# Kernel tuning notes

Hardware: AMD Instinct MI355X
Metric: run time of the kernel (lower is better)

Reference implementation:

```python
import jax, jax.numpy as jnp
import numpy as np

N_NODES = 50000
N_EDGES = 800000
C_IN = 64
C_HID = 64
C_OUT = 64


def _glorot(key, shape):
    lim = (6.0 / (shape[0] + shape[1])) ** 0.5
    return jax.random.uniform(key, shape, jnp.float32, -lim, lim)


def setup_inputs() -> dict:
    key = jax.random.key(0)
    ks = jax.random.split(key, 8)
    x = jax.random.normal(ks[0], (N_NODES, C_IN), jnp.float32)
    edge_index = jax.random.randint(ks[1], (2, N_EDGES), 0, N_NODES, jnp.int64)
    return {
        "x": x,
        "edge_index": edge_index,
        # ChebConv layer 1 (K=2): lins[0], lins[1], bias
        "W1_0": _glorot(ks[2], (C_IN, C_HID)),
        "W1_1": _glorot(ks[3], (C_IN, C_HID)),
        "b1": jnp.zeros((C_HID,), jnp.float32),
        # ChebConv layer 2 (K=2)
        "W2_0": _glorot(ks[4], (C_HID, C_OUT)),
        "W2_1": _glorot(ks[5], (C_HID, C_OUT)),
        "b2": jnp.zeros((C_OUT,), jnp.float32),
    }


def _lhat_matvec(x, src, dst, num_nodes):
    """Apply scaled Laplacian L_hat = -D^{-1/2} A D^{-1/2} (PyG ChebConv,
    sym norm, lambda_max=2; diagonal cancels exactly)."""
    ones = jnp.ones(src.shape[0], x.dtype)
    deg = jnp.zeros(num_nodes, x.dtype).at[src].add(ones)
    dis = jnp.where(deg > 0, deg ** -0.5, 0.0)  # deg_inv_sqrt, inf -> 0
    w = -(dis[src] * dis[dst])                  # per-edge weight
    # gather source features, scale, scatter-add to destinations
    return jnp.zeros_like(x).at[dst].add(w[:, None] * x[src])


def reference(x, edge_index, W1_0, W1_1, b1, W2_0, W2_1, b2):
    src, dst = edge_index[0], edge_index[1]
    n = x.shape[0]
    # ChebConv 1: T0 = x, T1 = L_hat x
    h = x @ W1_0 + _lhat_matvec(x, src, dst, n) @ W1_1 + b1
    h = jax.nn.relu(h)
    # ChebConv 2
    out = h @ W2_0 + _lhat_matvec(h, src, dst, n) @ W2_1 + b2
    return out
```

## Files before the change

### kernel.cpp

```cpp
#include <hip/hip_runtime.h>
#include <hip/hip_bf16.h>

#define NN 50000
#define NE 800000
#define C  64
#define CAP 56
#define NTILE (NN / 16)
#define HW 12500
#define EB 128
#define EC (NE / EB)
#define QB (EB / 4)
#define CONVB 782

typedef __attribute__((ext_vector_type(4))) float f32x4;
typedef __attribute__((ext_vector_type(8))) short s16x8;

__device__ __forceinline__ float ldv(const void* p, int i, int mode) {
    return mode ? __bfloat162float(((const __hip_bfloat16*)p)[i])
                : ((const float*)p)[i];
}
__device__ __forceinline__ float bflo(unsigned u) { return __uint_as_float(u << 16); }
__device__ __forceinline__ float bfhi(unsigned u) { return __uint_as_float(u & 0xffff0000u); }
__device__ __forceinline__ unsigned f2bf(float f) {
    __hip_bfloat16 h = __float2bfloat16(f);
    return (unsigned)*reinterpret_cast<unsigned short*>(&h);
}
__device__ __forceinline__ int detect_i64(const int* __restrict__ ei) {
    int z = 0;
#pragma unroll
    for (int k = 0; k < 8; ++k) z += (ei[2 * k + 1] == 0);
    return z == 8;
}
__device__ __forceinline__ int detect_bf16(const unsigned* __restrict__ xw) {
    int hits = 0;
#pragma unroll
    for (int k = 0; k < 16; ++k) {
        unsigned hb = (xw[k] >> 8) & 0x7Fu;
        hits += (hb >= 0x37u && hb <= 0x41u);
    }
    return hits >= 8;
}

__device__ __forceinline__ void lded2(const int* __restrict__ ei, int e, int i64,
                                      int& s0, int& s1, int& d0, int& d1) {
    if (i64) {
        int4 sv = *(const int4*)(ei + 2 * e);
        int4 dv = *(const int4*)(ei + 2 * (NE + e));
        s0 = sv.x; s1 = sv.z; d0 = dv.x; d1 = dv.z;
    } else {
        int2 sv = *(const int2*)(ei + e);
        int2 dv = *(const int2*)(ei + NE + e);
        s0 = sv.x; s1 = sv.y; d0 = dv.x; d1 = dv.y;
    }
}

__global__ void __launch_bounds__(1024) histconv_kernel(
        const int* __restrict__ ei, const void* __restrict__ x,
        const void* W10, const void* W11, const void* W20, const void* W21,
        const void* b1, const void* b2,
        unsigned* __restrict__ srcp, unsigned* __restrict__ dstp,
        unsigned short* __restrict__ xb,
        __hip_bfloat16* __restrict__ wbf, float* __restrict__ biasf) {
    extern __shared__ unsigned sh[];
    int b = blockIdx.x, t = threadIdx.x;
    if (b < EB) {
        for (int i = t; i < 2 * HW; i += 1024) sh[i] = 0u;
        __syncthreads();
        int i64 = detect_i64(ei);
        int base = b * EC;
        for (int p = t; p < EC / 2; p += 1024) {
            int e = base + 2 * p;
            int s0, s1, d0, d1;
            lded2(ei, e, i64, s0, s1, d0, d1);
            atomicAdd(&sh[s0 >> 2], 1u << (8 * (s0 & 3)));
            atomicAdd(&sh[s1 >> 2], 1u << (8 * (s1 & 3)));
            atomicAdd(&sh[HW + (d0 >> 2)], 1u << (8 * (d0 & 3)));
            atomicAdd(&sh[HW + (d1 >> 2)], 1u << (8 * (d1 & 3)));
        }
        __syncthreads();
        unsigned* so = srcp + b * HW;
        unsigned* dd = dstp + b * HW;
        for (int i = t; i < HW; i += 1024) { so[i] = sh[i]; dd[i] = sh[HW + i]; }
    } else if (b < EB + CONVB) {
        int m = detect_bf16((const unsigned*)x);
        int i4 = (b - EB) * 1024 + t;
        if (i4 < NN * C / 4) {
            if (m) {
                ((uint2*)xb)[i4] = ((const uint2*)x)[i4];
            } else {
                float4 v = ((const float4*)x)[i4];
                uint2 o;
                o.x = (f2bf(v.y) << 16) | f2bf(v.x);
                o.y = (f2bf(v.w) << 16) | f2bf(v.z);
                ((uint2*)xb)[i4] = o;
            }
        }
    } else if (b < EB + CONVB + 4) {
        int m = detect_bf16((const unsigned*)x);
        int wi = b - EB - CONVB;
        const void* src = (wi == 0) ? W10 : (wi == 1) ? W11 : (wi == 2) ? W20 : W21;
        for (int i = t; i < C * C; i += 1024)
            wbf[wi * C * C + i] = __float2bfloat16(ldv(src, i, m));
    } else {
        int m = detect_bf16((const unsigned*)x);
        if (t < 2 * C) biasf[t] = ldv((t < C) ? b1 : b2, t & (C - 1), m);
    }
}

__global__ void offs_kernel(const unsigned* __restrict__ srcp, unsigned* __restrict__ dstp,
                            float* __restrict__ dis, unsigned* __restrict__ pcnt) {
    int t = blockIdx.x * blockDim.x + threadIdx.x;
    if (t < 4 * HW) {
        int w = t >> 2, c = t & 3;
        unsigned c0 = 0, c1 = 0, c2 = 0, c3 = 0;
        for (int b = c * QB; b < c * QB + QB; ++b) {
            unsigned v = srcp[b * HW + w];
            c0 += v & 255u; c1 += (v >> 8) & 255u; c2 += (v >> 16) & 255u; c3 += v >> 24;
        }
        c0 += __shfl_xor(c0, 1); c0 += __shfl_xor(c0, 2);
        c1 += __shfl_xor(c1, 1); c1 += __shfl_xor(c1, 2);
        c2 += __shfl_xor(c2, 1); c2 += __shfl_xor(c2, 2);
        c3 += __shfl_xor(c3, 1); c3 += __shfl_xor(c3, 2);
        if (c == 0) {
            float4 o;
            o.x = c0 ? rsqrtf((float)c0) : 0.f;
            o.y = c1 ? rsqrtf((float)c1) : 0.f;
            o.z = c2 ? rsqrtf((float)c2) : 0.f;
            o.w = c3 ? rsqrtf((float)c3) : 0.f;
            ((float4*)dis)[w] = o;
        }
    } else if (t < 8 * HW) {
        int u = t - 4 * HW;
        int w = u >> 2, c = u & 3;
        int b0 = c * QB;
        unsigned l0 = 0, l1 = 0, l2 = 0, l3 = 0;
        for (int b = b0; b < b0 + QB; ++b) {
            unsigned v = dstp[b * HW + w];
            l0 += v & 255u; l1 += (v >> 8) & 255u; l2 += (v >> 16) & 255u; l3 += v >> 24;
        }
        unsigned i0 = l0, i1 = l1, i2 = l2, i3 = l3, p;
        p = __shfl_up(i0, 1, 4); if (c >= 1) i0 += p;
        p = __shfl_up(i0, 2, 4); if (c >= 2) i0 += p;
        p = __shfl_up(i1, 1, 4); if (c >= 1) i1 += p;
        p = __shfl_up(i1, 2, 4); if (c >= 2) i1 += p;
        p = __shfl_up(i2, 1, 4); if (c >= 1) i2 += p;
        p = __shfl_up(i2, 2, 4); if (c >= 2) i2 += p;
        p = __shfl_up(i3, 1, 4); if (c >= 1) i3 += p;
        p = __shfl_up(i3, 2, 4); if (c >= 2) i3 += p;
        unsigned r0 = i0 - l0, r1 = i1 - l1, r2 = i2 - l2, r3 = i3 - l3;
        for (int b = b0; b < b0 + QB; ++b) {
            unsigned v = dstp[b * HW + w];
            dstp[b * HW + w] = r0 | (r1 << 8) | (r2 << 16) | (r3 << 24);
            r0 += v & 255u; r1 += (v >> 8) & 255u; r2 += (v >> 16) & 255u; r3 += v >> 24;
        }
        if (c == 3) {
            uint4 pc; pc.x = r0; pc.y = r1; pc.z = r2; pc.w = r3;
            ((uint4*)pcnt)[w] = pc;
        }
    }
}

__global__ void __launch_bounds__(1024) build_kernel(const int* __restrict__ ei,
                                                     const unsigned* __restrict__ dstp,
                                                     const float* __restrict__ dis,
                                                     unsigned* __restrict__ pairs) {
    extern __shared__ unsigned sh[];
    unsigned* cnt = sh;
    unsigned* off = sh + HW;
    int t = threadIdx.x;
    const unsigned* my = dstp + blockIdx.x * HW;
    for (int i = t; i < HW; i += 1024) { cnt[i] = 0u; off[i] = my[i]; }
    __syncthreads();
    int i64 = detect_i64(ei);
    int base = blockIdx.x * EC;
    for (int p = t; p < EC / 2; p += 1024) {
        int e = base + 2 * p;
        int s0, s1, d0, d1;
        lded2(ei, e, i64, s0, s1, d0, d1);
        unsigned sh0 = 8 * (d0 & 3), sh1 = 8 * (d1 & 3);
        unsigned old0 = atomicAdd(&cnt[d0 >> 2], 1u << sh0);
        unsigned w0 = ((old0 >> sh0) & 255u) + ((off[d0 >> 2] >> sh0) & 255u);
        if (w0 < CAP) pairs[d0 * CAP + w0] = (unsigned)s0 | (f2bf(dis[s0]) << 16);
        unsigned old1 = atomicAdd(&cnt[d1 >> 2], 1u << sh1);
        unsigned w1 = ((old1 >> sh1) & 255u) + ((off[d1 >> 2] >> sh1) & 255u);
        if (w1 < CAP) pairs[d1 * CAP + w1] = (unsigned)s1 | (f2bf(dis[s1]) << 16);
    }
}

__device__ __forceinline__ void acc8(float* a, float w, uint4 f) {
    a[0] += w * bflo(f.x);  a[1] += w * bfhi(f.x);
    a[2] += w * bflo(f.y);  a[3] += w * bfhi(f.y);
    a[4] += w * bflo(f.z);  a[5] += w * bfhi(f.z);
    a[6] += w * bflo(f.w);  a[7] += w * bfhi(f.w);
}
__global__ void gather_kernel(const unsigned short* __restrict__ xb,
                              unsigned short* __restrict__ y,
                              const unsigned* __restrict__ pcnt,
                              const unsigned* __restrict__ pairs,
                              const float* __restrict__ dis) {
    int wave = threadIdx.x >> 6, lane = threadIdx.x & 63;
    int g = lane >> 3, l8 = lane & 7;
    int r = (blockIdx.x * 4 + wave) * 8 + g;
    if (r >= NN) return;
    unsigned n = pcnt[r];
    if (n > CAP) n = CAP;
    const unsigned* pp = pairs + (unsigned)r * CAP;
    float a[8];
#pragma unroll
    for (int k = 0; k < 8; ++k) a[k] = 0.f;
    for (unsigned j = 0; j < n; j += 4) {
        uint4 q = *(const uint4*)(pp + j);
        int   s0 = q.x & 0xFFFF, s1 = q.y & 0xFFFF, s2 = q.z & 0xFFFF, s3 = q.w & 0xFFFF;
        float w0 = bfhi(q.x), w1 = bfhi(q.y), w2 = bfhi(q.z), w3 = bfhi(q.w);
        if (j + 1 >= n) { s1 = 0; w1 = 0.f; }
        if (j + 2 >= n) { s2 = 0; w2 = 0.f; }
        if (j + 3 >= n) { s3 = 0; w3 = 0.f; }
        uint4 f0 = *(const uint4*)(xb + s0 * C + l8 * 8);
        uint4 f1 = *(const uint4*)(xb + s1 * C + l8 * 8);
        uint4 f2 = *(const uint4*)(xb + s2 * C + l8 * 8);
        uint4 f3 = *(const uint4*)(xb + s3 * C + l8 * 8);
        acc8(a, w0, f0); acc8(a, w1, f1); acc8(a, w2, f2); acc8(a, w3, f3);
    }
    float sc = -dis[r];
    uint4 o;
    o.x = (f2bf(a[1] * sc) << 16) | f2bf(a[0] * sc);
    o.y = (f2bf(a[3] * sc) << 16) | f2bf(a[2] * sc);
    o.z = (f2bf(a[5] * sc) << 16) | f2bf(a[4] * sc);
    o.w = (f2bf(a[7] * sc) << 16) | f2bf(a[6] * sc);
    *(uint4*)(y + r * C + l8 * 8) = o;
}

template <bool RELU>
__global__ void gemm_kernel(const __hip_bfloat16* __restrict__ xb,
                            const __hip_bfloat16* __restrict__ y,
                            const __hip_bfloat16* __restrict__ wb,
                            const float* __restrict__ biasf,
                            void* __restrict__ out,
                            const unsigned* __restrict__ xorig) {
    int wave = threadIdx.x >> 6, lane = threadIdx.x & 63;
    int q = lane >> 4, n15 = lane & 15;
    const short* W0 = (const short*)wb;
    const short* W1 = (const short*)(wb + C * C);
    int out_bf16 = detect_bf16(xorig);

    s16x8 bf[4][4];
    for (int c = 0; c < 4; ++c)
        for (int t = 0; t < 4; ++t) {
            const short* W = (t < 2) ? W0 : W1;
            int rowbase = (t & 1) * 32 + q * 8;
            s16x8 v;
#pragma unroll
            for (int j = 0; j < 8; ++j) v[j] = W[(rowbase + j) * C + c * 16 + n15];
            bf[c][t] = v;
        }
    float bias0[4];
    for (int c = 0; c < 4; ++c) bias0[c] = biasf[c * 16 + n15];

    for (int tile = blockIdx.x * 4 + wave; tile < NTILE; tile += gridDim.x * 4) {
        int nb = tile * 16;
        f32x4 acc[4];
#pragma unroll
        for (int c = 0; c < 4; ++c) acc[c] = (f32x4){0.f, 0.f, 0.f, 0.f};
#pragma unroll
        for (int t = 0; t < 4; ++t) {
            const short* src = (t < 2) ? (const short*)xb : (const short*)y;
            s16x8 a = *(const s16x8*)(src + (nb + n15) * C + (t & 1) * 32 + q * 8);
#pragma unroll
            for (int c = 0; c < 4; ++c)
                acc[c] = __builtin_amdgcn_mfma_f32_16x16x32_bf16(a, bf[c][t], acc[c], 0, 0, 0);
        }
        if (out_bf16) {
            __hip_bfloat16* o = (__hip_bfloat16*)out;
#pragma unroll
            for (int c = 0; c < 4; ++c)
#pragma unroll
                for (int i = 0; i < 4; ++i) {
                    float v = acc[c][i] + bias0[c];
                    if (RELU) v = fmaxf(v, 0.f);
                    o[(nb + q * 4 + i) * C + c * 16 + n15] = __float2bfloat16(v);
                }
        } else {
            float* o = (float*)out;
#pragma unroll
            for (int c = 0; c < 4; ++c)
#pragma unroll
                for (int i = 0; i < 4; ++i) {
                    float v = acc[c][i] + bias0[c];
                    if (RELU) v = fmaxf(v, 0.f);
                    o[(nb + q * 4 + i) * C + c * 16 + n15] = v;
                }
        }
    }
}

template <bool RELU>
__global__ void gemm_kernel_bf16out(const __hip_bfloat16* __restrict__ xb,
                                    const __hip_bfloat16* __restrict__ y,
                                    const __hip_bfloat16* __restrict__ wb,
                                    const float* __restrict__ biasf,
                                    __hip_bfloat16* __restrict__ o) {
    int wave = threadIdx.x >> 6, lane = threadIdx.x & 63;
    int q = lane >> 4, n15 = lane & 15;
    const short* W0 = (const short*)wb;
    const short* W1 = (const short*)(wb + C * C);
    s16x8 bf[4][4];
    for (int c = 0; c < 4; ++c)
        for (int t = 0; t < 4; ++t) {
            const short* W = (t < 2) ? W0 : W1;
            int rowbase = (t & 1) * 32 + q * 8;
            s16x8 v;
#pragma unroll
            for (int j = 0; j < 8; ++j) v[j] = W[(rowbase + j) * C + c * 16 + n15];
            bf[c][t] = v;
        }
    float bias0[4];
    for (int c = 0; c < 4; ++c) bias0[c] = biasf[c * 16 + n15];

    for (int tile = blockIdx.x * 4 + wave; tile < NTILE; tile += gridDim.x * 4) {
        int nb = tile * 16;
        f32x4 acc[4];
#pragma unroll
        for (int c = 0; c < 4; ++c) acc[c] = (f32x4){0.f, 0.f, 0.f, 0.f};
#pragma unroll
        for (int t = 0; t < 4; ++t) {
            const short* src = (t < 2) ? (const short*)xb : (const short*)y;
            s16x8 a = *(const s16x8*)(src + (nb + n15) * C + (t & 1) * 32 + q * 8);
#pragma unroll
            for (int c = 0; c < 4; ++c)
                acc[c] = __builtin_amdgcn_mfma_f32_16x16x32_bf16(a, bf[c][t], acc[c], 0, 0, 0);
        }
#pragma unroll
        for (int c = 0; c < 4; ++c)
#pragma unroll
            for (int i = 0; i < 4; ++i) {
                float v = acc[c][i] + bias0[c];
                if (RELU) v = fmaxf(v, 0.f);
                o[(nb + q * 4 + i) * C + c * 16 + n15] = __float2bfloat16(v);
            }
    }
}

extern "C" void kernel_launch(void* const* d_in, const int* in_sizes, int n_in,
                              void* d_out, int out_size, void* d_ws, size_t ws_size,
                              hipStream_t stream) {
    const void* x    = d_in[0];
    const int*  ei   = (const int*)d_in[1];
    const void* W1_0 = d_in[2];
    const void* W1_1 = d_in[3];
    const void* b1   = d_in[4];
    const void* W2_0 = d_in[5];
    const void* W2_1 = d_in[6];
    const void* b2   = d_in[7];

    char* ws = (char*)d_ws;
    float*    dis   = (float*)(ws + 4096);
    unsigned* pcnt  = (unsigned*)(ws + 208896);
    float*    biasf = (float*)(ws + 413696);
    __hip_bfloat16* wbf = (__hip_bfloat16*)(ws + 414208);
    unsigned* pairs = (unsigned*)(ws + 450560);
    unsigned short* xb = (unsigned short*)(ws + 11651072);
    unsigned short* y  = (unsigned short*)(ws + 18051072);
    __hip_bfloat16* h  = (__hip_bfloat16*)(ws + 24451072);
    unsigned* srcp  = (unsigned*)(ws + 30851072);
    unsigned* dstp  = (unsigned*)(ws + 37251072);

    histconv_kernel<<<EB + CONVB + 5, 1024, 2 * HW * 4, stream>>>(
        ei, x, W1_0, W1_1, W2_0, W2_1, b1, b2, srcp, dstp, xb, wbf, biasf);
    offs_kernel<<<(8 * HW + 255) / 256, 256, 0, stream>>>(srcp, dstp, dis, pcnt);
    build_kernel<<<EB, 1024, 2 * HW * 4, stream>>>(ei, dstp, dis, pairs);

    gather_kernel<<<(NN + 31) / 32, 256, 0, stream>>>(xb, y, pcnt, pairs, dis);
    gemm_kernel_bf16out<true><<<782, 256, 0, stream>>>((const __hip_bfloat16*)xb,
                                                       (const __hip_bfloat16*)y, wbf, biasf, h);

    gather_kernel<<<(NN + 31) / 32, 256, 0, stream>>>((const unsigned short*)h, y, pcnt, pairs, dis);
    gemm_kernel<false><<<782, 256, 0, stream>>>(h, (const __hip_bfloat16*)y,
                                                wbf + 2 * C * C, biasf + C, d_out,
                                                (const unsigned*)x);
}
```

Baseline: 172.7 us.

## Fuse neighbor gather with MFMA GEMM per 64-node tile via shared memory

```diff
diff --git a/kernel.cpp b/kernel.cpp
--- a/kernel.cpp
+++ b/kernel.cpp
@@ -5,12 +5,12 @@
 #define NE 800000
 #define C  64
 #define CAP 56
-#define NTILE (NN / 16)
 #define HW 12500
 #define EB 128
 #define EC (NE / EB)
 #define QB (EB / 4)
 #define CONVB 782
+#define YST 72
 
 typedef __attribute__((ext_vector_type(4))) float f32x4;
 typedef __attribute__((ext_vector_type(8))) short s16x8;
@@ -193,58 +193,66 @@
     a[4] += w * bflo(f.z);  a[5] += w * bfhi(f.z);
     a[6] += w * bflo(f.w);  a[7] += w * bfhi(f.w);
 }
-__global__ void gather_kernel(const unsigned short* __restrict__ xb,
-                              unsigned short* __restrict__ y,
-                              const unsigned* __restrict__ pcnt,
-                              const unsigned* __restrict__ pairs,
-                              const float* __restrict__ dis) {
+template <bool RELU, bool OUT_DYN>
+__global__ void __launch_bounds__(256) fused_kernel(
+        const unsigned short* __restrict__ xb,
+        const unsigned* __restrict__ pcnt,
+        const unsigned* __restrict__ pairs,
+        const float* __restrict__ dis,
+        const __hip_bfloat16* __restrict__ wb,
+        const float* __restrict__ biasf,
+        void* __restrict__ out,
+        const unsigned* __restrict__ xorig) {
+    __shared__ unsigned short yt[64 * YST];
     int wave = threadIdx.x >> 6, lane = threadIdx.x & 63;
     int g = lane >> 3, l8 = lane & 7;
-    int r = (blockIdx.x * 4 + wave) * 8 + g;
-    if (r >= NN) return;
-    unsigned n = pcnt[r];
-    if (n > CAP) n = CAP;
-    const unsigned* pp = pairs + (unsigned)r * CAP;
-    float a[8];
-#pragma unroll
-    for (int k = 0; k < 8; ++k) a[k] = 0.f;
-    for (unsigned j = 0; j < n; j += 4) {
-        uint4 q = *(const uint4*)(pp + j);
-        int   s0 = q.x & 0xFFFF, s1 = q.y & 0xFFFF, s2 = q.z & 0xFFFF, s3 = q.w & 0xFFFF;
-        float w0 = bfhi(q.x), w1 = bfhi(q.y), w2 = bfhi(q.z), w3 = bfhi(q.w);
-        if (j + 1 >= n) { s1 = 0; w1 = 0.f; }
-        if (j + 2 >= n) { s2 = 0; w2 = 0.f; }
-        if (j + 3 >= n) { s3 = 0; w3 = 0.f; }
-        uint4 f0 = *(const uint4*)(xb + s0 * C + l8 * 8);
-        uint4 f1 = *(const uint4*)(xb + s1 * C + l8 * 8);
-        uint4 f2 = *(const uint4*)(xb + s2 * C + l8 * 8);
-        uint4 f3 = *(const uint4*)(xb + s3 * C + l8 * 8);
-        acc8(a, w0, f0); acc8(a, w1, f1); acc8(a, w2, f2); acc8(a, w3, f3);
-    }
-    float sc = -dis[r];
-    uint4 o;
-    o.x = (f2bf(a[1] * sc) << 16) | f2bf(a[0] * sc);
-    o.y = (f2bf(a[3] * sc) << 16) | f2bf(a[2] * sc);
-    o.z = (f2bf(a[5] * sc) << 16) | f2bf(a[4] * sc);
-    o.w = (f2bf(a[7] * sc) << 16) | f2bf(a[6] * sc);
-    *(uint4*)(y + r * C + l8 * 8) = o;
-}
-
-template <bool RELU>
-__global__ void gemm_kernel(const __hip_bfloat16* __restrict__ xb,
-                            const __hip_bfloat16* __restrict__ y,
-                            const __hip_bfloat16* __restrict__ wb,
-                            const float* __restrict__ biasf,
-                            void* __restrict__ out,
-                            const unsigned* __restrict__ xorig) {
-    int wave = threadIdx.x >> 6, lane = threadIdx.x & 63;
+    int nb0 = blockIdx.x * 64;
+
+#pragma unroll
+    for (int pass = 0; pass < 2; ++pass) {
+        int local = wave * 16 + pass * 8 + g;
+        int r = nb0 + local;
+        if (r < NN) {
+            unsigned n = pcnt[r];
+            if (n > CAP) n = CAP;
+            const unsigned* pp = pairs + (unsigned)r * CAP;
+            float a[8];
+#pragma unroll
+            for (int k = 0; k < 8; ++k) a[k] = 0.f;
+            for (unsigned j = 0; j < n; j += 4) {
+                uint4 q = *(const uint4*)(pp + j);
+                int   s0 = q.x & 0xFFFF, s1 = q.y & 0xFFFF, s2 = q.z & 0xFFFF, s3 = q.w & 0xFFFF;
+                float w0 = bfhi(q.x), w1 = bfhi(q.y), w2 = bfhi(q.z), w3 = bfhi(q.w);
+                if (j + 1 >= n) { s1 = 0; w1 = 0.f; }
+                if (j + 2 >= n) { s2 = 0; w2 = 0.f; }
+                if (j + 3 >= n) { s3 = 0; w3 = 0.f; }
+                uint4 f0 = *(const uint4*)(xb + s0 * C + l8 * 8);
+                uint4 f1 = *(const uint4*)(xb + s1 * C + l8 * 8);
+                uint4 f2 = *(const uint4*)(xb + s2 * C + l8 * 8);
+                uint4 f3 = *(const uint4*)(xb + s3 * C + l8 * 8);
+                acc8(a, w0, f0); acc8(a, w1, f1); acc8(a, w2, f2); acc8(a, w3, f3);
+            }
+            float sc = -dis[r];
+            uint4 o;
+            o.x = (f2bf(a[1] * sc) << 16) | f2bf(a[0] * sc);
+            o.y = (f2bf(a[3] * sc) << 16) | f2bf(a[2] * sc);
+            o.z = (f2bf(a[5] * sc) << 16) | f2bf(a[4] * sc);
+            o.w = (f2bf(a[7] * sc) << 16) | f2bf(a[6] * sc);
+            *(uint4*)(yt + local * YST + l8 * 8) = o;
+        } else {
+            uint4 z = {0u, 0u, 0u, 0u};
+            *(uint4*)(yt + local * YST + l8 * 8) = z;
+        }
+    }
+    __syncthreads();
+
     int q = lane >> 4, n15 = lane & 15;
     const short* W0 = (const short*)wb;
     const short* W1 = (const short*)(wb + C * C);
-    int out_bf16 = detect_bf16(xorig);
-
     s16x8 bf[4][4];
+#pragma unroll
     for (int c = 0; c < 4; ++c)
+#pragma unroll
         for (int t = 0; t < 4; ++t) {
             const short* W = (t < 2) ? W0 : W1;
             int rowbase = (t & 1) * 32 + q * 8;
@@ -253,90 +261,49 @@
             for (int j = 0; j < 8; ++j) v[j] = W[(rowbase + j) * C + c * 16 + n15];
             bf[c][t] = v;
         }
-    float bias0[4];
-    for (int c = 0; c < 4; ++c) bias0[c] = biasf[c * 16 + n15];
-
-    for (int tile = blockIdx.x * 4 + wave; tile < NTILE; tile += gridDim.x * 4) {
-        int nb = tile * 16;
-        f32x4 acc[4];
-#pragma unroll
-        for (int c = 0; c < 4; ++c) acc[c] = (f32x4){0.f, 0.f, 0.f, 0.f};
-#pragma unroll
-        for (int t = 0; t < 4; ++t) {
-            const short* src = (t < 2) ? (const short*)xb : (const short*)y;
-            s16x8 a = *(const s16x8*)(src + (nb + n15) * C + (t & 1) * 32 + q * 8);
-#pragma unroll
-            for (int c = 0; c < 4; ++c)
-                acc[c] = __builtin_amdgcn_mfma_f32_16x16x32_bf16(a, bf[c][t], acc[c], 0, 0, 0);
-        }
-        if (out_bf16) {
-            __hip_bfloat16* o = (__hip_bfloat16*)out;
-#pragma unroll
-            for (int c = 0; c < 4; ++c)
-#pragma unroll
-                for (int i = 0; i < 4; ++i) {
-                    float v = acc[c][i] + bias0[c];
-                    if (RELU) v = fmaxf(v, 0.f);
-                    o[(nb + q * 4 + i) * C + c * 16 + n15] = __float2bfloat16(v);
-                }
+    int nb = nb0 + wave * 16;
+    f32x4 acc[4];
+#pragma unroll
+    for (int c = 0; c < 4; ++c) acc[c] = (f32x4){0.f, 0.f, 0.f, 0.f};
+#pragma unroll
+    for (int t = 0; t < 4; ++t) {
+        s16x8 a;
+        if (t < 2) {
+            a = *(const s16x8*)((const short*)xb + (nb + n15) * C + (t & 1) * 32 + q * 8);
         } else {
-            float* o = (float*)out;
-#pragma unroll
-            for (int c = 0; c < 4; ++c)
-#pragma unroll
-                for (int i = 0; i < 4; ++i) {
-                    float v = acc[c][i] + bias0[c];
-                    if (RELU) v = fmaxf(v, 0.f);
-                    o[(nb + q * 4 + i) * C + c * 16 + n15] = v;
-                }
-        }
-    }
-}
-
-template <bool RELU>
-__global__ void gemm_kernel_bf16out(const __hip_bfloat16* __restrict__ xb,
-                                    const __hip_bfloat16* __restrict__ y,
-                                    const __hip_bfloat16* __restrict__ wb,
-                                    const float* __restrict__ biasf,
-                                    __hip_bfloat16* __restrict__ o) {
-    int wave = threadIdx.x >> 6, lane = threadIdx.x & 63;
-    int q = lane >> 4, n15 = lane & 15;
-    const short* W0 = (const short*)wb;
-    const short* W1 = (const short*)(wb + C * C);
-    s16x8 bf[4][4];
-    for (int c = 0; c < 4; ++c)
-        for (int t = 0; t < 4; ++t) {
-            const short* W = (t < 2) ? W0 : W1;
-            int rowbase = (t & 1) * 32 + q * 8;
-            s16x8 v;
-#pragma unroll
-            for (int j = 0; j < 8; ++j) v[j] = W[(rowbase + j) * C + c * 16 + n15];
-            bf[c][t] = v;
-        }
-    float bias0[4];
-    for (int c = 0; c < 4; ++c) bias0[c] = biasf[c * 16 + n15];
-
-    for (int tile = blockIdx.x * 4 + wave; tile < NTILE; tile += gridDim.x * 4) {
-        int nb = tile * 16;
-        f32x4 acc[4];
-#pragma unroll
-        for (int c = 0; c < 4; ++c) acc[c] = (f32x4){0.f, 0.f, 0.f, 0.f};
-#pragma unroll
-        for (int t = 0; t < 4; ++t) {
-            const short* src = (t < 2) ? (const short*)xb : (const short*)y;
-            s16x8 a = *(const s16x8*)(src + (nb + n15) * C + (t & 1) * 32 + q * 8);
-#pragma unroll
-            for (int c = 0; c < 4; ++c)
-                acc[c] = __builtin_amdgcn_mfma_f32_16x16x32_bf16(a, bf[c][t], acc[c], 0, 0, 0);
+            a = *(const s16x8*)((const short*)yt + (wave * 16 + n15) * YST + (t & 1) * 32 + q * 8);
         }
 #pragma unroll
         for (int c = 0; c < 4; ++c)
+            acc[c] = __builtin_amdgcn_mfma_f32_16x16x32_bf16(a, bf[c][t], acc[c], 0, 0, 0);
+    }
+    int out_bf16 = OUT_DYN ? detect_bf16(xorig) : 1;
+    if (out_bf16) {
+        __hip_bfloat16* o = (__hip_bfloat16*)out;
+#pragma unroll
+        for (int c = 0; c < 4; ++c) {
+            float bias0 = biasf[c * 16 + n15];
 #pragma unroll
             for (int i = 0; i < 4; ++i) {
-                float v = acc[c][i] + bias0[c];
+                int row = nb + q * 4 + i;
+                float v = acc[c][i] + bias0;
                 if (RELU) v = fmaxf(v, 0.f);
-                o[(nb + q * 4 + i) * C + c * 16 + n15] = __float2bfloat16(v);
+                if (row < NN) o[row * C + c * 16 + n15] = __float2bfloat16(v);
             }
+        }
+    } else {
+        float* o = (float*)out;
+#pragma unroll
+        for (int c = 0; c < 4; ++c) {
+            float bias0 = biasf[c * 16 + n15];
+#pragma unroll
+            for (int i = 0; i < 4; ++i) {
+                int row = nb + q * 4 + i;
+                float v = acc[c][i] + bias0;
+                if (RELU) v = fmaxf(v, 0.f);
+                if (row < NN) o[row * C + c * 16 + n15] = v;
+            }
+        }
     }
 }
 
@@ -359,22 +326,19 @@
     __hip_bfloat16* wbf = (__hip_bfloat16*)(ws + 414208);
     unsigned* pairs = (unsigned*)(ws + 450560);
     unsigned short* xb = (unsigned short*)(ws + 11651072);
-    unsigned short* y  = (unsigned short*)(ws + 18051072);
-    __hip_bfloat16* h  = (__hip_bfloat16*)(ws + 24451072);
-    unsigned* srcp  = (unsigned*)(ws + 30851072);
-    unsigned* dstp  = (unsigned*)(ws + 37251072);
+    __hip_bfloat16* h  = (__hip_bfloat16*)(ws + 18051072);
+    unsigned* srcp  = (unsigned*)(ws + 24451072);
+    unsigned* dstp  = (unsigned*)(ws + 30851072);
 
     histconv_kernel<<<EB + CONVB + 5, 1024, 2 * HW * 4, stream>>>(
         ei, x, W1_0, W1_1, W2_0, W2_1, b1, b2, srcp, dstp, xb, wbf, biasf);
     offs_kernel<<<(8 * HW + 255) / 256, 256, 0, stream>>>(srcp, dstp, dis, pcnt);
     build_kernel<<<EB, 1024, 2 * HW * 4, stream>>>(ei, dstp, dis, pairs);
 
-    gather_kernel<<<(NN + 31) / 32, 256, 0, stream>>>(xb, y, pcnt, pairs, dis);
-    gemm_kernel_bf16out<true><<<782, 256, 0, stream>>>((const __hip_bfloat16*)xb,
-                                                       (const __hip_bfloat16*)y, wbf, biasf, h);
-
-    gather_kernel<<<(NN + 31) / 32, 256, 0, stream>>>((const unsigned short*)h, y, pcnt, pairs, dis);
-    gemm_kernel<false><<<782, 256, 0, stream>>>(h, (const __hip_bfloat16*)y,
-                                                wbf + 2 * C * C, biasf + C, d_out,
-                                                (const unsigned*)x);
-}
+    fused_kernel<true, false><<<(NN + 63) / 64, 256, 0, stream>>>(
+        xb, pcnt, pairs, dis, wbf, biasf, h, (const unsigned*)x);
+
+    fused_kernel<false, true><<<(NN + 63) / 64, 256, 0, stream>>>(
+        (const unsigned short*)h, pcnt, pairs, dis, wbf + 2 * C * C, biasf + C, d_out,
+        (const unsigned*)x);
+}
```

Result: faster. 159.5 us (-7.6%).
